# Performance work log

Hardware: AMD Instinct MI355X
Metric: run time of the kernel (lower is better)

The kernel has to match this reference:

```python
import jax, jax.numpy as jnp
import numpy as np

B, C, D, H, W = 2, 3, 128, 192, 192
# spacing = (1, 1, 1) -> unit spacing, so jnp.gradient default is exact


def setup_inputs() -> dict:
    key = jax.random.key(0)
    # small displacements keep det(I + du) > 0 so log(det) is finite
    x = jax.random.normal(key, (B, C, D, H, W), dtype=jnp.float32) * 0.05
    return {"x": x}


def _jacobian_log_det_sq(x):
    # torch.gradient == numpy-style gradient: central differences in the
    # interior, one-sided differences at the boundaries.
    eye = jnp.eye(3, dtype=x.dtype)
    rows = []
    for j in range(3):  # derivative along spatial axis j (D, H, W)
        g = jnp.gradient(x, axis=2 + j)          # (B, C, D, H, W) = du_i/dx_j
        g = jnp.moveaxis(g, 1, -1)               # (B, D, H, W, i)
        rows.append(g + eye[j])                  # add delta_ij (identity)
    # J[..., j, i] = du_i/dx_j + delta_ij ; det is transpose-invariant
    J = jnp.stack(rows, axis=-2)                 # (B, D, H, W, 3, 3)
    det = jnp.linalg.det(J)                      # (B, D, H, W)
    return jnp.log(det) ** 2


def reference(x):
    return _jacobian_log_det_sq(x)
```

## Files before the change

kernel.cpp:

```cpp
#include <hip/hip_runtime.h>

constexpr int B = 2, C = 3, D = 128, H = 192, W = 192;
constexpr int sH = W;
constexpr int sD = H * W;
constexpr int sC = D * H * W;
constexpr int sB = C * sC;

constexpr int TH = 16;
constexpr int TW = 16;
constexpr int DC = 8;
constexpr int HX = H / TH;
constexpr int WX = (W / 4) / TW;
constexpr int NDC = D / DC;
constexpr int NB = B * NDC * HX * WX;
constexpr int ROWS = TH + 2;
constexpr int RSTR = TW + 1;
constexpr int CH_STR = ROWS * RSTR;
constexpr int BUFSZ = C * CH_STR;

__global__ __launch_bounds__(256, 4) void jac_logdet_sq(
    const float* __restrict__ x, float* __restrict__ out) {
    __shared__ float4 lds[2][BUFSZ];

    const int tid = threadIdx.x;
    const int tx = tid & 15;
    const int ty = tid >> 4;

    int bb = blockIdx.x;
    const int wx = bb % WX; bb /= WX;
    const int hx = bb % HX; bb /= HX;
    const int dch = bb % NDC;
    const int b = bb / NDC;

    const int d0 = dch * DC;
    const int h0 = hx * TH;
    const int h = h0 + ty;
    const int w0 = (wx * TW + tx) * 4;

    const float* pb = x + b * sB;
    const int cidx = h * sH + w0;

    const int hc = tid / 32;
    const int hr = (tid >> 4) & 1;
    const int htx = tid & 15;
    const int hh = hr ? ((h0 + TH < H) ? h0 + TH : H - 1)
                      : ((h0 > 0) ? h0 - 1 : 0);
    const int hidx = hh * sH + (wx * TW + htx) * 4;
    const int hlds = hc * CH_STR + (hr ? (TH + 1) : 0) * RSTR + htx;

    const float chc = (h > 0 && h < H - 1) ? 0.5f : 1.0f;

    float4 cm[3], c0[3], cp[3], cn[3];
    float4 hv0, hvp, hvn;
    float lg[3], rg[3], lgn[3], rgn[3];

    const int dm = (d0 > 0) ? d0 - 1 : 0;
#pragma unroll
    for (int c = 0; c < 3; ++c) {
        c0[c] = *(const float4*)(pb + c * sC + d0 * sD + cidx);
        cm[c] = *(const float4*)(pb + c * sC + dm * sD + cidx);
        cp[c] = *(const float4*)(pb + c * sC + (d0 + 1) * sD + cidx);
    }
    if (tid < 96) {
        hv0 = *(const float4*)(pb + hc * sC + d0 * sD + hidx);
        hvp = *(const float4*)(pb + hc * sC + (d0 + 1) * sD + hidx);
    }
    if (tx == 0 && w0 > 0) {
#pragma unroll
        for (int c = 0; c < 3; ++c) lg[c] = pb[c * sC + d0 * sD + cidx - 1];
    }
    if (tx == 15 && w0 + 4 < W) {
#pragma unroll
        for (int c = 0; c < 3; ++c) rg[c] = pb[c * sC + d0 * sD + cidx + 4];
    }
#pragma unroll
    for (int c = 0; c < 3; ++c)
        lds[0][c * CH_STR + (ty + 1) * RSTR + tx] = c0[c];
    if (tid < 96) lds[0][hlds] = hv0;
    __syncthreads();

    int obase = ((b * D + d0) * H + h) * W + w0;

#pragma unroll
    for (int dd = 0; dd < DC; ++dd) {
        const int d = d0 + dd;
        const float cdc = (d > 0 && d < D - 1) ? 0.5f : 1.0f;
        const float4* bufc = lds[dd & 1];

        float gd[3][4], gh[3][4], gw[3][4];
#pragma unroll
        for (int c = 0; c < 3; ++c) {
            gd[c][0] = (cp[c].x - cm[c].x) * cdc;
            gd[c][1] = (cp[c].y - cm[c].y) * cdc;
            gd[c][2] = (cp[c].z - cm[c].z) * cdc;
            gd[c][3] = (cp[c].w - cm[c].w) * cdc;
        }

        if (dd < DC - 1) {
            const int dpp = (d + 2 < D) ? d + 2 : D - 1;
#pragma unroll
            for (int c = 0; c < 3; ++c)
                cn[c] = *(const float4*)(pb + c * sC + dpp * sD + cidx);
            if (dd < DC - 2 && tid < 96)
                hvn = *(const float4*)(pb + hc * sC + dpp * sD + hidx);
            if (tx == 0 && w0 > 0) {
#pragma unroll
                for (int c = 0; c < 3; ++c)
                    lgn[c] = pb[c * sC + (d + 1) * sD + cidx - 1];
            }
            if (tx == 15 && w0 + 4 < W) {
#pragma unroll
                for (int c = 0; c < 3; ++c)
                    rgn[c] = pb[c * sC + (d + 1) * sD + cidx + 4];
            }
        }

#pragma unroll
        for (int c = 0; c < 3; ++c) {
            const float4 hp = bufc[c * CH_STR + (ty + 2) * RSTR + tx];
            const float4 hm = bufc[c * CH_STR + (ty    ) * RSTR + tx];
            gh[c][0] = (hp.x - hm.x) * chc;
            gh[c][1] = (hp.y - hm.y) * chc;
            gh[c][2] = (hp.z - hm.z) * chc;
            gh[c][3] = (hp.w - hm.w) * chc;

            const float lft = (tx == 0) ? lg[c]
                : bufc[c * CH_STR + (ty + 1) * RSTR + tx - 1].w;
            const float rgt = (tx == 15) ? rg[c]
                : bufc[c * CH_STR + (ty + 1) * RSTR + tx + 1].x;
            gw[c][0] = (w0 == 0)     ? (c0[c].y - c0[c].x)
                                     : 0.5f * (c0[c].y - lft);
            gw[c][1] = 0.5f * (c0[c].z - c0[c].x);
            gw[c][2] = 0.5f * (c0[c].w - c0[c].y);
            gw[c][3] = (w0 + 4 == W) ? (c0[c].w - c0[c].z)
                                     : 0.5f * (rgt - c0[c].z);
        }

        float r[4];
#pragma unroll
        for (int e = 0; e < 4; ++e) {
            const float a00 = gd[0][e] + 1.0f, a01 = gd[1][e], a02 = gd[2][e];
            const float a10 = gh[0][e], a11 = gh[1][e] + 1.0f, a12 = gh[2][e];
            const float a20 = gw[0][e], a21 = gw[1][e], a22 = gw[2][e] + 1.0f;
            const float det = a00 * (a11 * a22 - a12 * a21)
                            - a01 * (a10 * a22 - a12 * a20)
                            + a02 * (a10 * a21 - a11 * a20);
            const float l = __logf(det);
            r[e] = l * l;
        }
        *(float4*)(out + obase) = make_float4(r[0], r[1], r[2], r[3]);
        obase += sD;

        if (dd < DC - 1) {
#pragma unroll
            for (int c = 0; c < 3; ++c)
                lds[(dd + 1) & 1][c * CH_STR + (ty + 1) * RSTR + tx] = cp[c];
            if (tid < 96) lds[(dd + 1) & 1][hlds] = hvp;
            __syncthreads();

#pragma unroll
            for (int c = 0; c < 3; ++c) {
                cm[c] = c0[c]; c0[c] = cp[c]; cp[c] = cn[c];
                lg[c] = lgn[c]; rg[c] = rgn[c];
            }
            hvp = hvn;
        }
    }
}

extern "C" void kernel_launch(void* const* d_in, const int* in_sizes, int n_in,
                              void* d_out, int out_size, void* d_ws, size_t ws_size,
                              hipStream_t stream) {
    const float* x = (const float*)d_in[0];
    float* out = (float*)d_out;
    jac_logdet_sq<<<dim3(NB), dim3(256), 0, stream>>>(x, out);
}
```

Measured before the change: 178.4 us.

## Tile full image rows per block to drop W-direction halo loads

Each block now covers the full width (48 float4 columns) and 8 rows with 384 threads, in place of a 16x16 float4 tile. Because the tile spans the whole row, the left and right neighbours along W always come from shared memory, so the per-slice scalar global halo loads and their registers are removed. The H-halo is loaded by 288 threads, and the ratio of halo to interior shrinks in W but grows in H (2 halo rows per 8). The larger block and LDS footprint may lower occupancy.

```diff
diff --git a/kernel.cpp b/kernel.cpp
--- a/kernel.cpp
+++ b/kernel.cpp
@@ -6,28 +6,27 @@
 constexpr int sC = D * H * W;
 constexpr int sB = C * sC;
 
-constexpr int TH = 16;
-constexpr int TW = 16;
+constexpr int THREADS = 384;
+constexpr int TH = 8;
+constexpr int TWQ = W / 4;
 constexpr int DC = 8;
 constexpr int HX = H / TH;
-constexpr int WX = (W / 4) / TW;
 constexpr int NDC = D / DC;
-constexpr int NB = B * NDC * HX * WX;
+constexpr int NB = B * NDC * HX;
 constexpr int ROWS = TH + 2;
-constexpr int RSTR = TW + 1;
+constexpr int RSTR = TWQ + 1;
 constexpr int CH_STR = ROWS * RSTR;
 constexpr int BUFSZ = C * CH_STR;
 
-__global__ __launch_bounds__(256, 4) void jac_logdet_sq(
+__global__ __launch_bounds__(THREADS, 4) void jac_logdet_sq(
     const float* __restrict__ x, float* __restrict__ out) {
     __shared__ float4 lds[2][BUFSZ];
 
     const int tid = threadIdx.x;
-    const int tx = tid & 15;
-    const int ty = tid >> 4;
+    const int tx = tid % TWQ;
+    const int ty = tid / TWQ;
 
     int bb = blockIdx.x;
-    const int wx = bb % WX; bb /= WX;
     const int hx = bb % HX; bb /= HX;
     const int dch = bb % NDC;
     const int b = bb / NDC;
@@ -35,24 +34,25 @@
     const int d0 = dch * DC;
     const int h0 = hx * TH;
     const int h = h0 + ty;
-    const int w0 = (wx * TW + tx) * 4;
+    const int w0 = tx * 4;
 
     const float* pb = x + b * sB;
     const int cidx = h * sH + w0;
 
-    const int hc = tid / 32;
-    const int hr = (tid >> 4) & 1;
-    const int htx = tid & 15;
-    const int hh = hr ? ((h0 + TH < H) ? h0 + TH : H - 1)
-                      : ((h0 > 0) ? h0 - 1 : 0);
-    const int hidx = hh * sH + (wx * TW + htx) * 4;
-    const int hlds = hc * CH_STR + (hr ? (TH + 1) : 0) * RSTR + htx;
+    const int hc = tid / 96;
+    const int hrem = tid % 96;
+    const int hrr = hrem / TWQ;
+    const int htx = hrem % TWQ;
+    const int hh = hrr ? ((h0 + TH < H) ? h0 + TH : H - 1)
+                       : ((h0 > 0) ? h0 - 1 : 0);
+    const int hidx = hh * sH + htx * 4;
+    const int hlds = hc * CH_STR + (hrr ? (TH + 1) : 0) * RSTR + htx;
+    const bool halo = (tid < 288);
 
     const float chc = (h > 0 && h < H - 1) ? 0.5f : 1.0f;
 
     float4 cm[3], c0[3], cp[3], cn[3];
     float4 hv0, hvp, hvn;
-    float lg[3], rg[3], lgn[3], rgn[3];
 
     const int dm = (d0 > 0) ? d0 - 1 : 0;
 #pragma unroll
@@ -61,22 +61,14 @@
         cm[c] = *(const float4*)(pb + c * sC + dm * sD + cidx);
         cp[c] = *(const float4*)(pb + c * sC + (d0 + 1) * sD + cidx);
     }
-    if (tid < 96) {
+    if (halo) {
         hv0 = *(const float4*)(pb + hc * sC + d0 * sD + hidx);
         hvp = *(const float4*)(pb + hc * sC + (d0 + 1) * sD + hidx);
-    }
-    if (tx == 0 && w0 > 0) {
-#pragma unroll
-        for (int c = 0; c < 3; ++c) lg[c] = pb[c * sC + d0 * sD + cidx - 1];
-    }
-    if (tx == 15 && w0 + 4 < W) {
-#pragma unroll
-        for (int c = 0; c < 3; ++c) rg[c] = pb[c * sC + d0 * sD + cidx + 4];
     }
 #pragma unroll
     for (int c = 0; c < 3; ++c)
         lds[0][c * CH_STR + (ty + 1) * RSTR + tx] = c0[c];
-    if (tid < 96) lds[0][hlds] = hv0;
+    if (halo) lds[0][hlds] = hv0;
     __syncthreads();
 
     int obase = ((b * D + d0) * H + h) * W + w0;
@@ -101,18 +93,8 @@
 #pragma unroll
             for (int c = 0; c < 3; ++c)
                 cn[c] = *(const float4*)(pb + c * sC + dpp * sD + cidx);
-            if (dd < DC - 2 && tid < 96)
+            if (dd < DC - 2 && halo)
                 hvn = *(const float4*)(pb + hc * sC + dpp * sD + hidx);
-            if (tx == 0 && w0 > 0) {
-#pragma unroll
-                for (int c = 0; c < 3; ++c)
-                    lgn[c] = pb[c * sC + (d + 1) * sD + cidx - 1];
-            }
-            if (tx == 15 && w0 + 4 < W) {
-#pragma unroll
-                for (int c = 0; c < 3; ++c)
-                    rgn[c] = pb[c * sC + (d + 1) * sD + cidx + 4];
-            }
         }
 
 #pragma unroll
@@ -124,16 +106,16 @@
             gh[c][2] = (hp.z - hm.z) * chc;
             gh[c][3] = (hp.w - hm.w) * chc;
 
-            const float lft = (tx == 0) ? lg[c]
-                : bufc[c * CH_STR + (ty + 1) * RSTR + tx - 1].w;
-            const float rgt = (tx == 15) ? rg[c]
-                : bufc[c * CH_STR + (ty + 1) * RSTR + tx + 1].x;
-            gw[c][0] = (w0 == 0)     ? (c0[c].y - c0[c].x)
-                                     : 0.5f * (c0[c].y - lft);
+            const int txl = (tx > 0) ? tx - 1 : tx;
+            const int txr = (tx < TWQ - 1) ? tx + 1 : tx;
+            const float lft = bufc[c * CH_STR + (ty + 1) * RSTR + txl].w;
+            const float rgt = bufc[c * CH_STR + (ty + 1) * RSTR + txr].x;
+            gw[c][0] = (tx == 0)       ? (c0[c].y - c0[c].x)
+                                       : 0.5f * (c0[c].y - lft);
             gw[c][1] = 0.5f * (c0[c].z - c0[c].x);
             gw[c][2] = 0.5f * (c0[c].w - c0[c].y);
-            gw[c][3] = (w0 + 4 == W) ? (c0[c].w - c0[c].z)
-                                     : 0.5f * (rgt - c0[c].z);
+            gw[c][3] = (tx == TWQ - 1) ? (c0[c].w - c0[c].z)
+                                       : 0.5f * (rgt - c0[c].z);
         }
 
         float r[4];
@@ -155,13 +137,12 @@
 #pragma unroll
             for (int c = 0; c < 3; ++c)
                 lds[(dd + 1) & 1][c * CH_STR + (ty + 1) * RSTR + tx] = cp[c];
-            if (tid < 96) lds[(dd + 1) & 1][hlds] = hvp;
+            if (halo) lds[(dd + 1) & 1][hlds] = hvp;
             __syncthreads();
 
 #pragma unroll
             for (int c = 0; c < 3; ++c) {
                 cm[c] = c0[c]; c0[c] = cp[c]; cp[c] = cn[c];
-                lg[c] = lgn[c]; rg[c] = rgn[c];
             }
             hvp = hvn;
         }
@@ -173,5 +154,5 @@
                               hipStream_t stream) {
     const float* x = (const float*)d_in[0];
     float* out = (float*)d_out;
-    jac_logdet_sq<<<dim3(NB), dim3(256), 0, stream>>>(x, out);
+    jac_logdet_sq<<<dim3(NB), dim3(THREADS), 0, stream>>>(x, out);
 }
```

New measurement: 176.2 us. No clear change (-1.2%).
